# Optimization experiments

Hardware: AMD Instinct MI355X
Metric: run time of the kernel (lower is better)

The kernel has to match this reference:

```python
import jax, jax.numpy as jnp
import numpy as np

E = 16   # num_experts
K = 4    # num_activated_experts
B, S, H, I = 4, 1024, 1024, 2048


def setup_inputs() -> dict:
    key = jax.random.key(0)
    k0, k1, k2, k3 = jax.random.split(key, 4)
    scale = 0.02
    return {
        "hidden_states": jax.random.normal(k0, (B, S, H), jnp.float32),
        "router_w": jax.random.normal(k1, (H, E), jnp.float32) * scale,
        "router_b": jnp.zeros((E,), jnp.float32),
        "w1": jax.random.normal(k2, (E, H, I), jnp.float32) * scale,
        "b1": jnp.zeros((E, I), jnp.float32),
        "w2": jax.random.normal(k3, (E, I, H), jnp.float32) * scale,
        "b2": jnp.zeros((E, H), jnp.float32),
    }


def reference(hidden_states, router_w, router_b, w1, b1, w2, b2):
    b, s, h = hidden_states.shape
    # router: softmax over experts, pick top-k, renormalize top-k weights
    logits = hidden_states @ router_w + router_b            # [B,S,E]
    probs = jax.nn.softmax(logits, axis=-1)
    topw, topi = jax.lax.top_k(probs, K)                    # [B,S,K]
    topw = topw / jnp.sum(topw, axis=-1, keepdims=True)
    # scatter top-k weights into dense per-expert combine weights [B,S,E]
    combine = jnp.sum(
        jax.nn.one_hot(topi, E, dtype=hidden_states.dtype) * topw[..., None],
        axis=2,
    )
    x = hidden_states.reshape(b * s, h)                     # [T,H]
    c = combine.reshape(b * s, E)                           # [T,E]

    def body(acc, expert):
        w1e, b1e, w2e, b2e, ce = expert
        hmid = jax.nn.gelu(x @ w1e + b1e, approximate=False)  # [T,I]
        return acc + (hmid @ w2e + b2e) * ce[:, None], None

    out, _ = jax.lax.scan(body, jnp.zeros_like(x), (w1, b1, w2, b2, c.T))
    return out.reshape(b, s, h)
```

## Files before the change

kernel.cpp:

```cpp
#include <hip/hip_runtime.h>

#define T_TOK 4096
#define H_DIM 1024
#define I_DIM 2048
#define E_NUM 16
#define K_TOP 4
#define BM 128
#define BK 32
#define MAX_TILES 144
#define PAD_PAIRS (MAX_TILES * BM)
#define RW_Q 4104

typedef __attribute__((ext_vector_type(8))) short s16x8;
typedef __attribute__((ext_vector_type(4))) float f32x4;
typedef __attribute__((ext_vector_type(4))) unsigned short u16x4;
typedef __attribute__((ext_vector_type(8))) unsigned short u16x8;

__device__ __forceinline__ unsigned short f2bf(float f) {
  unsigned u = __float_as_uint(f);
  u += 0x7fffu + ((u >> 16) & 1u);
  return (unsigned short)(u >> 16);
}

__device__ __forceinline__ void mfma_bf16(const s16x8& a, const s16x8& b, f32x4& c) {
  asm("v_mfma_f32_16x16x32_bf16 %0, %1, %2, %0" : "+v"(c) : "v"(a), "v"(b));
}

__device__ __forceinline__ void gld16(const void* g, void* l) {
  __builtin_amdgcn_global_load_lds(
      (const __attribute__((address_space(1))) unsigned int*)g,
      (__attribute__((address_space(3))) unsigned int*)l, 16, 0, 0);
}

__global__ __launch_bounds__(256) void cvt_kernel(const float* __restrict__ x,
                                                  unsigned short* __restrict__ xb) {
  size_t i = ((size_t)blockIdx.x * 256 + threadIdx.x) * 8;
  f32x4 a = *(const f32x4*)(x + i);
  f32x4 b = *(const f32x4*)(x + i + 4);
  u16x8 o;
  o[0] = f2bf(a[0]); o[1] = f2bf(a[1]); o[2] = f2bf(a[2]); o[3] = f2bf(a[3]);
  o[4] = f2bf(b[0]); o[5] = f2bf(b[1]); o[6] = f2bf(b[2]); o[7] = f2bf(b[3]);
  *(u16x8*)(xb + i) = o;
}

__global__ __launch_bounds__(256) void router_kernel(
    const float* __restrict__ x, const float* __restrict__ rw,
    const float* __restrict__ rb, int* __restrict__ topi,
    float* __restrict__ topw, int* __restrict__ counts) {
  __shared__ float rws[4 * RW_Q];
  const int tid = threadIdx.x;
  for (int idx = tid * 4; idx < H_DIM * E_NUM; idx += 256 * 4) {
    f32x4 v = *(const f32x4*)(rw + idx);
    int h = idx >> 4, e0 = idx & 15;
    *(f32x4*)&rws[(h >> 8) * RW_Q + (h & 255) * 16 + e0] = v;
  }
  __syncthreads();
  const int w = tid >> 6, l = tid & 63;
  const int e = l & 15, q = l >> 4;
  const float rbe = rb[e];
  const float* ldsb = &rws[q * RW_Q + e];
#pragma unroll
  for (int i = 0; i < 4; ++i) {
    const int t = blockIdx.x * 16 + w * 4 + i;
    const float* xr = x + (size_t)t * H_DIM + (q << 8);
    float acc = 0.f;
#pragma unroll 8
    for (int hh = 0; hh < 256; hh += 4) {
      f32x4 xv = *(const f32x4*)(xr + hh);
      acc += xv[0] * ldsb[(hh + 0) * 16];
      acc += xv[1] * ldsb[(hh + 1) * 16];
      acc += xv[2] * ldsb[(hh + 2) * 16];
      acc += xv[3] * ldsb[(hh + 3) * 16];
    }
    acc += __shfl_xor(acc, 16);
    acc += __shfl_xor(acc, 32);
    float logit = acc + rbe;
    float m = logit;
    m = fmaxf(m, __shfl_xor(m, 1));
    m = fmaxf(m, __shfl_xor(m, 2));
    m = fmaxf(m, __shfl_xor(m, 4));
    m = fmaxf(m, __shfl_xor(m, 8));
    float ex = expf(logit - m);
    int rank = 0;
    const int b16 = l & 48;
#pragma unroll
    for (int j = 0; j < 16; ++j) {
      float vj = __shfl(ex, b16 + j);
      rank += (vj > ex) || (vj == ex && j < e);
    }
    float sel = (rank < K_TOP) ? ex : 0.f;
    float subs = sel;
    subs += __shfl_xor(subs, 1);
    subs += __shfl_xor(subs, 2);
    subs += __shfl_xor(subs, 4);
    subs += __shfl_xor(subs, 8);
    if (q == 0 && rank < K_TOP) {
      topi[t * K_TOP + rank] = e;
      topw[t * K_TOP + rank] = ex / subs;
      atomicAdd(&counts[e], 1);
    }
  }
}

__global__ void scan_kernel(const int* __restrict__ counts, int* padBase,
                            int* tileExpert, int* tileStart, int* nTiles,
                            int* cursor) {
  if (threadIdx.x != 0 || blockIdx.x != 0) return;
  int base = 0, nt = 0;
  for (int e = 0; e < E_NUM; ++e) {
    padBase[e] = base;
    cursor[e] = 0;
    int tc = (counts[e] + BM - 1) >> 7;
    for (int i = 0; i < tc; ++i) {
      tileExpert[nt] = e;
      tileStart[nt] = base + (i << 7);
      ++nt;
    }
    base += tc << 7;
  }
  nTiles[0] = nt;
}

__global__ __launch_bounds__(256) void scatter_kernel(
    const int* __restrict__ topi, const float* __restrict__ topw,
    const int* __restrict__ padBase, int* __restrict__ cursor,
    int* __restrict__ pairTok, float* __restrict__ pairW,
    int* __restrict__ pairPos) {
  int t = blockIdx.x * 256 + threadIdx.x;
  if (t >= T_TOK) return;
#pragma unroll
  for (int k = 0; k < K_TOP; ++k) {
    int e = topi[t * K_TOP + k];
    int pos = atomicAdd(&cursor[e], 1);
    int idx = padBase[e] + pos;
    pairTok[idx] = t;
    pairW[idx] = topw[t * K_TOP + k];
    pairPos[t * K_TOP + k] = idx;
  }
}

__global__ __launch_bounds__(256) void transpose_kernel(
    const float* __restrict__ src, unsigned short* __restrict__ dst, int R,
    int C) {
  size_t es = (size_t)R * C;
  src += es * blockIdx.z;
  dst += es * blockIdx.z;
  int r0 = blockIdx.y * 64, c0 = blockIdx.x * 64;
  __shared__ float tle[64][65];
  int rr = threadIdx.x >> 4, cc = (threadIdx.x & 15) * 4;
#pragma unroll
  for (int i = 0; i < 4; ++i) {
    f32x4 v = *(const f32x4*)(src + (size_t)(r0 + rr + 16 * i) * C + c0 + cc);
    tle[rr + 16 * i][cc + 0] = v[0];
    tle[rr + 16 * i][cc + 1] = v[1];
    tle[rr + 16 * i][cc + 2] = v[2];
    tle[rr + 16 * i][cc + 3] = v[3];
  }
  __syncthreads();
#pragma unroll
  for (int i = 0; i < 4; ++i) {
    int oc = c0 + rr + 16 * i;
    u16x4 o;
    o[0] = f2bf(tle[cc + 0][rr + 16 * i]);
    o[1] = f2bf(tle[cc + 1][rr + 16 * i]);
    o[2] = f2bf(tle[cc + 2][rr + 16 * i]);
    o[3] = f2bf(tle[cc + 3][rr + 16 * i]);
    *(u16x4*)(dst + (size_t)oc * R + r0 + cc) = o;
  }
}

__global__ __launch_bounds__(256, 4) void gemm1_kernel(
    const unsigned short* __restrict__ xb, const unsigned short* __restrict__ w1t,
    const float* __restrict__ b1, unsigned short* __restrict__ hmid,
    const int* __restrict__ pairTok, const int* __restrict__ tileExpert,
    const int* __restrict__ tileStart, const int* __restrict__ nTiles) {
  const int bid = blockIdx.x;
  const int lin = (bid & 7) * ((16 * MAX_TILES) >> 3) + (bid >> 3);
  const int tx = lin & 15, ty = lin >> 4;
  if (ty >= nTiles[0]) return;
  const int e = tileExpert[ty];
  const int tsp = tileStart[ty];
  const int n0 = tx * 128;
  __shared__ unsigned short As[2][BM * BK];
  __shared__ unsigned short Bs[2][BM * BK];
  const int tid = threadIdx.x, w = tid >> 6, l = tid & 63;
  const int rbase = w * 16 + (l >> 2);
  const int segp = (l & 3) ^ ((l >> 3) & 3);
  int tok0 = pairTok[tsp + rbase];
  if (tok0 < 0) tok0 = 0;
  int tok1 = pairTok[tsp + rbase + 64];
  if (tok1 < 0) tok1 = 0;
  const char* gA0 = (const char*)(xb + (size_t)tok0 * H_DIM) + segp * 16;
  const char* gA1 = (const char*)(xb + (size_t)tok1 * H_DIM) + segp * 16;
  const unsigned short* wbase = w1t + (size_t)e * I_DIM * H_DIM;
  const char* gB0 = (const char*)(wbase + (size_t)(n0 + rbase) * H_DIM) + segp * 16;
  const char* gB1 = (const char*)(wbase + (size_t)(n0 + rbase + 64) * H_DIM) + segp * 16;

  f32x4 acc[4][4];
#pragma unroll
  for (int m = 0; m < 4; ++m)
#pragma unroll
    for (int n = 0; n < 4; ++n) acc[m][n] = f32x4{0.f, 0.f, 0.f, 0.f};

  const int wr = w >> 1, wc = w & 1, lrow = l & 15, g = l >> 4;
  const int gs = g ^ ((l >> 1) & 3);
  const int NK = H_DIM / BK;

  gld16(gA0, &As[0][w * 512]);
  gld16(gA1, &As[0][2048 + w * 512]);
  gld16(gB0, &Bs[0][w * 512]);
  gld16(gB1, &Bs[0][2048 + w * 512]);

  for (int kt = 0; kt < NK; ++kt) {
    __syncthreads();
    if (kt + 1 < NK) {
      const int kb = (kt + 1) * 64;
      const int nb = (kt + 1) & 1;
      gld16(gA0 + kb, &As[nb][w * 512]);
      gld16(gA1 + kb, &As[nb][2048 + w * 512]);
      gld16(gB0 + kb, &Bs[nb][w * 512]);
      gld16(gB1 + kb, &Bs[nb][2048 + w * 512]);
    }
    const int cb = kt & 1;
    const s16x8* Ap = (const s16x8*)As[cb];
    const s16x8* Bp = (const s16x8*)Bs[cb];
    s16x8 av[4], bv[4];
#pragma unroll
    for (int m = 0; m < 4; ++m) av[m] = Ap[(wr * 64 + m * 16 + lrow) * 4 + gs];
#pragma unroll
    for (int n = 0; n < 4; ++n) bv[n] = Bp[(wc * 64 + n * 16 + lrow) * 4 + gs];
#pragma unroll
    for (int m = 0; m < 4; ++m)
#pragma unroll
      for (int n = 0; n < 4; ++n) mfma_bf16(av[m], bv[n], acc[m][n]);
  }

  const float* b1e = b1 + (size_t)e * I_DIM;
#pragma unroll
  for (int m = 0; m < 4; ++m) {
    const int rw0 = wr * 64 + m * 16 + g * 4;
#pragma unroll
    for (int n = 0; n < 4; ++n) {
      const int col = n0 + wc * 64 + n * 16 + lrow;
      const float bb = b1e[col];
      f32x4 v = acc[m][n];
#pragma unroll
      for (int j = 0; j < 4; ++j) {
        const int p = tsp + rw0 + j;
        float xv = v[j] + bb;
        float y = 0.7978845608028654f * (xv + 0.044715f * xv * xv * xv);
        float ey = __expf(2.f * y);
        float th = 1.f - 2.f / (ey + 1.f);
        float ge = 0.5f * xv * (1.f + th);
        hmid[(size_t)p * I_DIM + col] = f2bf(ge);
      }
    }
  }
}

__global__ __launch_bounds__(256, 4) void gemm2_kernel(
    const unsigned short* __restrict__ hmid,
    const unsigned short* __restrict__ w2t, const float* __restrict__ b2,
    float* __restrict__ out, unsigned short* __restrict__ pairOut,
    const int* __restrict__ pairTok, const float* __restrict__ pairW,
    const int* __restrict__ tileExpert, const int* __restrict__ tileStart,
    const int* __restrict__ nTiles, int usePairOut) {
  const int bid = blockIdx.x;
  const int lin = (bid & 7) * ((8 * MAX_TILES) >> 3) + (bid >> 3);
  const int tx = lin & 7, ty = lin >> 3;
  if (ty >= nTiles[0]) return;
  const int e = tileExpert[ty];
  const int tsp = tileStart[ty];
  const int n0 = tx * 128;
  __shared__ unsigned short As[2][BM * BK];
  __shared__ unsigned short Bs[2][BM * BK];
  const int tid = threadIdx.x, w = tid >> 6, l = tid & 63;
  const int rbase = w * 16 + (l >> 2);
  const int segp = (l & 3) ^ ((l >> 3) & 3);
  const char* gA0 = (const char*)(hmid + (size_t)(tsp + rbase) * I_DIM) + segp * 16;
  const char* gA1 = (const char*)(hmid + (size_t)(tsp + rbase + 64) * I_DIM) + segp * 16;
  const unsigned short* wbase = w2t + (size_t)e * H_DIM * I_DIM;
  const char* gB0 = (const char*)(wbase + (size_t)(n0 + rbase) * I_DIM) + segp * 16;
  const char* gB1 = (const char*)(wbase + (size_t)(n0 + rbase + 64) * I_DIM) + segp * 16;

  f32x4 acc[4][4];
#pragma unroll
  for (int m = 0; m < 4; ++m)
#pragma unroll
    for (int n = 0; n < 4; ++n) acc[m][n] = f32x4{0.f, 0.f, 0.f, 0.f};

  const int wr = w >> 1, wc = w & 1, lrow = l & 15, g = l >> 4;
  const int gs = g ^ ((l >> 1) & 3);
  const int NK = I_DIM / BK;

  gld16(gA0, &As[0][w * 512]);
  gld16(gA1, &As[0][2048 + w * 512]);
  gld16(gB0, &Bs[0][w * 512]);
  gld16(gB1, &Bs[0][2048 + w * 512]);

  for (int kt = 0; kt < NK; ++kt) {
    __syncthreads();
    if (kt + 1 < NK) {
      const int kb = (kt + 1) * 64;
      const int nb = (kt + 1) & 1;
      gld16(gA0 + kb, &As[nb][w * 512]);
      gld16(gA1 + kb, &As[nb][2048 + w * 512]);
      gld16(gB0 + kb, &Bs[nb][w * 512]);
      gld16(gB1 + kb, &Bs[nb][2048 + w * 512]);
    }
    const int cb = kt & 1;
    const s16x8* Ap = (const s16x8*)As[cb];
    const s16x8* Bp = (const s16x8*)Bs[cb];
    s16x8 av[4], bv[4];
#pragma unroll
    for (int m = 0; m < 4; ++m) av[m] = Ap[(wr * 64 + m * 16 + lrow) * 4 + gs];
#pragma unroll
    for (int n = 0; n < 4; ++n) bv[n] = Bp[(wc * 64 + n * 16 + lrow) * 4 + gs];
#pragma unroll
    for (int m = 0; m < 4; ++m)
#pragma unroll
      for (int n = 0; n < 4; ++n) mfma_bf16(av[m], bv[n], acc[m][n]);
  }

  if (usePairOut) {
#pragma unroll
    for (int m = 0; m < 4; ++m) {
      const int rw0 = wr * 64 + m * 16 + g * 4;
#pragma unroll
      for (int n = 0; n < 4; ++n) {
        const int col = n0 + wc * 64 + n * 16 + lrow;
        f32x4 v = acc[m][n];
#pragma unroll
        for (int j = 0; j < 4; ++j)
          pairOut[(size_t)(tsp + rw0 + j) * H_DIM + col] = f2bf(v[j]);
      }
    }
  } else {
    const float* b2e = b2 + (size_t)e * H_DIM;
#pragma unroll
    for (int m = 0; m < 4; ++m) {
      const int rw0 = wr * 64 + m * 16 + g * 4;
#pragma unroll
      for (int j = 0; j < 4; ++j) {
        const int p = tsp + rw0 + j;
        const int tok = pairTok[p];
        if (tok < 0) continue;
        const float pw = pairW[p];
        float* orow = out + (size_t)tok * H_DIM;
#pragma unroll
        for (int n = 0; n < 4; ++n) {
          const int col = n0 + wc * 64 + n * 16 + lrow;
          float val = (acc[m][n][j] + b2e[col]) * pw;
          atomicAdd(orow + col, val);
        }
      }
    }
  }
}

__global__ __launch_bounds__(256) void combine_kernel(
    const unsigned short* __restrict__ pairOut, const int* __restrict__ pairPos,
    const int* __restrict__ topi, const float* __restrict__ topw,
    const float* __restrict__ b2, float* __restrict__ out) {
  const int t = blockIdx.x * 2 + (threadIdx.x >> 7);
  const int c0 = (threadIdx.x & 127) * 8;
  float o[8];
#pragma unroll
  for (int j = 0; j < 8; ++j) o[j] = 0.f;
#pragma unroll
  for (int k = 0; k < K_TOP; ++k) {
    const int e = topi[t * K_TOP + k];
    const float pw = topw[t * K_TOP + k];
    const int pos = pairPos[t * K_TOP + k];
    u16x8 v = *(const u16x8*)(pairOut + (size_t)pos * H_DIM + c0);
    const float* b2r = b2 + (size_t)e * H_DIM + c0;
#pragma unroll
    for (int j = 0; j < 8; ++j) {
      float hv = __uint_as_float((unsigned)v[j] << 16);
      o[j] += pw * (hv + b2r[j]);
    }
  }
  float* orow = out + (size_t)t * H_DIM + c0;
  *(f32x4*)orow = f32x4{o[0], o[1], o[2], o[3]};
  *(f32x4*)(orow + 4) = f32x4{o[4], o[5], o[6], o[7]};
}

extern "C" void kernel_launch(void* const* d_in, const int* in_sizes, int n_in,
                              void* d_out, int out_size, void* d_ws,
                              size_t ws_size, hipStream_t stream) {
  const float* x = (const float*)d_in[0];
  const float* rw = (const float*)d_in[1];
  const float* rb = (const float*)d_in[2];
  const float* w1 = (const float*)d_in[3];
  const float* b1 = (const float*)d_in[4];
  const float* w2 = (const float*)d_in[5];
  const float* b2 = (const float*)d_in[6];
  float* out = (float*)d_out;
  char* ws = (char*)d_ws;

  const size_t xbSz = (size_t)T_TOK * H_DIM * 2;
  const size_t poSz = (size_t)PAD_PAIRS * H_DIM * 2;
  const size_t wtSz = (size_t)E_NUM * H_DIM * I_DIM * 2;
  const size_t hmSz = (size_t)PAD_PAIRS * I_DIM * 2;
  const size_t smallSz = (size_t)T_TOK * K_TOP * 4 * 3
                         + (size_t)PAD_PAIRS * 4 * 2
                         + 64 * 3 + MAX_TILES * 4 * 2 + 64;
  const size_t richTotal = poSz + wtSz + hmSz + smallSz;
  const size_t poorTotal = xbSz + wtSz + hmSz + smallSz;
  const int rich = ws_size >= richTotal;
  if (!rich && ws_size < poorTotal) return;

  size_t off = 0;
  unsigned short* xb = (unsigned short*)(ws + off);
  unsigned short* pairOut = (unsigned short*)(ws + off);
  off += rich ? poSz : xbSz;
  unsigned short* wT = (unsigned short*)(ws + off);
  off += wtSz;
  unsigned short* hmid = (unsigned short*)(ws + off);
  off += hmSz;
  int* topi = (int*)(ws + off);      off += (size_t)T_TOK * K_TOP * 4;
  float* topw = (float*)(ws + off);  off += (size_t)T_TOK * K_TOP * 4;
  int* pairPos = (int*)(ws + off);   off += (size_t)T_TOK * K_TOP * 4;
  int* pairTok = (int*)(ws + off);   off += (size_t)PAD_PAIRS * 4;
  float* pairW = (float*)(ws + off); off += (size_t)PAD_PAIRS * 4;
  int* counts = (int*)(ws + off);    off += 64;
  int* cursor = (int*)(ws + off);    off += 64;
  int* padBase = (int*)(ws + off);   off += 64;
  int* tileExpert = (int*)(ws + off); off += MAX_TILES * 4;
  int* tileStart = (int*)(ws + off);  off += MAX_TILES * 4;
  int* nTiles = (int*)(ws + off);     off += 64;

  hipMemsetAsync(counts, 0, 64, stream);
  hipMemsetAsync(pairTok, 0xFF, (size_t)PAD_PAIRS * 4, stream);
  if (!rich) hipMemsetAsync(out, 0, (size_t)T_TOK * H_DIM * 4, stream);

  cvt_kernel<<<T_TOK * H_DIM / (256 * 8), 256, 0, stream>>>(x, xb);
  router_kernel<<<T_TOK / 16, 256, 0, stream>>>(x, rw, rb, topi, topw, counts);
  scan_kernel<<<1, 64, 0, stream>>>(counts, padBase, tileExpert, tileStart,
                                    nTiles, cursor);
  scatter_kernel<<<T_TOK / 256, 256, 0, stream>>>(topi, topw, padBase, cursor,
                                                  pairTok, pairW, pairPos);
  transpose_kernel<<<dim3(I_DIM / 64, H_DIM / 64, E_NUM), 256, 0, stream>>>(
      w1, wT, H_DIM, I_DIM);
  gemm1_kernel<<<16 * MAX_TILES, 256, 0, stream>>>(
      xb, wT, b1, hmid, pairTok, tileExpert, tileStart, nTiles);
  transpose_kernel<<<dim3(H_DIM / 64, I_DIM / 64, E_NUM), 256, 0, stream>>>(
      w2, wT, I_DIM, H_DIM);
  gemm2_kernel<<<8 * MAX_TILES, 256, 0, stream>>>(
      hmid, wT, b2, out, pairOut, pairTok, pairW, tileExpert, tileStart, nTiles,
      rich);
  if (rich)
    combine_kernel<<<T_TOK / 2, 256, 0, stream>>>(pairOut, pairPos, topi, topw,
                                                  b2, out);
}
```

Measured before the change: 432.4 us.

## Drop scan kernel via inline tile mapping and split-K gemm2 into two partial buffers

Removes the single-thread scan kernel. Each gemm block and the scatter kernel now derive their expert and tile start directly from the expert counts, which saves one serial launch. When the workspace is large enough, gemm2 is split along K into two halves. Each half writes a bf16 partial result into its own buffer, and the combine kernel sums the two. This doubles the number of gemm2 blocks for better occupancy, at the cost of an extra partial-output write and read and an added bf16 rounding step.

Result: faster. 420.2 us (-2.8%).

```diff
diff --git a/kernel.cpp b/kernel.cpp
--- a/kernel.cpp
+++ b/kernel.cpp
@@ -30,6 +30,21 @@
   __builtin_amdgcn_global_load_lds(
       (const __attribute__((address_space(1))) unsigned int*)g,
       (__attribute__((address_space(3))) unsigned int*)l, 16, 0, 0);
+}
+
+__device__ __forceinline__ int tile_map(const int* counts, int ty, int* tsp) {
+  int e = -1, acc = 0, base = 0;
+#pragma unroll
+  for (int ee = 0; ee < E_NUM; ++ee) {
+    int tc = (counts[ee] + 127) >> 7;
+    if (ty >= acc && ty < acc + tc) {
+      e = ee;
+      *tsp = base + ((ty - acc) << 7);
+    }
+    acc += tc;
+    base += tc << 7;
+  }
+  return e;
 }
 
 __global__ __launch_bounds__(256) void cvt_kernel(const float* __restrict__ x,
@@ -102,30 +117,18 @@
   }
 }
 
-__global__ void scan_kernel(const int* __restrict__ counts, int* padBase,
-                            int* tileExpert, int* tileStart, int* nTiles,
-                            int* cursor) {
-  if (threadIdx.x != 0 || blockIdx.x != 0) return;
-  int base = 0, nt = 0;
-  for (int e = 0; e < E_NUM; ++e) {
-    padBase[e] = base;
-    cursor[e] = 0;
-    int tc = (counts[e] + BM - 1) >> 7;
-    for (int i = 0; i < tc; ++i) {
-      tileExpert[nt] = e;
-      tileStart[nt] = base + (i << 7);
-      ++nt;
-    }
-    base += tc << 7;
-  }
-  nTiles[0] = nt;
-}
-
 __global__ __launch_bounds__(256) void scatter_kernel(
     const int* __restrict__ topi, const float* __restrict__ topw,
-    const int* __restrict__ padBase, int* __restrict__ cursor,
+    const int* __restrict__ counts, int* __restrict__ cursor,
     int* __restrict__ pairTok, float* __restrict__ pairW,
     int* __restrict__ pairPos) {
+  int padBase[E_NUM];
+  int base = 0;
+#pragma unroll
+  for (int ee = 0; ee < E_NUM; ++ee) {
+    padBase[ee] = base;
+    base += ((counts[ee] + 127) >> 7) << 7;
+  }
   int t = blockIdx.x * 256 + threadIdx.x;
   if (t >= T_TOK) return;
 #pragma unroll
@@ -172,14 +175,13 @@
 __global__ __launch_bounds__(256, 4) void gemm1_kernel(
     const unsigned short* __restrict__ xb, const unsigned short* __restrict__ w1t,
     const float* __restrict__ b1, unsigned short* __restrict__ hmid,
-    const int* __restrict__ pairTok, const int* __restrict__ tileExpert,
-    const int* __restrict__ tileStart, const int* __restrict__ nTiles) {
+    const int* __restrict__ pairTok, const int* __restrict__ counts) {
   const int bid = blockIdx.x;
-  const int lin = (bid & 7) * ((16 * MAX_TILES) >> 3) + (bid >> 3);
+  const int lin = (bid & 7) * 288 + (bid >> 3);
   const int tx = lin & 15, ty = lin >> 4;
-  if (ty >= nTiles[0]) return;
-  const int e = tileExpert[ty];
-  const int tsp = tileStart[ty];
+  int tsp = 0;
+  const int e = tile_map(counts, ty, &tsp);
+  if (e < 0) return;
   const int n0 = tx * 128;
   __shared__ unsigned short As[2][BM * BK];
   __shared__ unsigned short Bs[2][BM * BK];
@@ -261,27 +263,34 @@
 __global__ __launch_bounds__(256, 4) void gemm2_kernel(
     const unsigned short* __restrict__ hmid,
     const unsigned short* __restrict__ w2t, const float* __restrict__ b2,
-    float* __restrict__ out, unsigned short* __restrict__ pairOut,
-    const int* __restrict__ pairTok, const float* __restrict__ pairW,
-    const int* __restrict__ tileExpert, const int* __restrict__ tileStart,
-    const int* __restrict__ nTiles, int usePairOut) {
+    float* __restrict__ out, unsigned short* __restrict__ poA,
+    unsigned short* __restrict__ poB, const int* __restrict__ pairTok,
+    const float* __restrict__ pairW, const int* __restrict__ counts, int mode) {
   const int bid = blockIdx.x;
-  const int lin = (bid & 7) * ((8 * MAX_TILES) >> 3) + (bid >> 3);
-  const int tx = lin & 7, ty = lin >> 3;
-  if (ty >= nTiles[0]) return;
-  const int e = tileExpert[ty];
-  const int tsp = tileStart[ty];
+  const int nchunk = (mode == 2) ? 288 : 144;
+  const int lin = (bid & 7) * nchunk + (bid >> 3);
+  const int kh = (mode == 2) ? (lin & 1) : 0;
+  const int tx = (mode == 2) ? ((lin >> 1) & 7) : (lin & 7);
+  const int ty = (mode == 2) ? (lin >> 4) : (lin >> 3);
+  int tsp = 0;
+  const int e = tile_map(counts, ty, &tsp);
+  if (e < 0) return;
   const int n0 = tx * 128;
   __shared__ unsigned short As[2][BM * BK];
   __shared__ unsigned short Bs[2][BM * BK];
   const int tid = threadIdx.x, w = tid >> 6, l = tid & 63;
   const int rbase = w * 16 + (l >> 2);
   const int segp = (l & 3) ^ ((l >> 3) & 3);
-  const char* gA0 = (const char*)(hmid + (size_t)(tsp + rbase) * I_DIM) + segp * 16;
-  const char* gA1 = (const char*)(hmid + (size_t)(tsp + rbase + 64) * I_DIM) + segp * 16;
+  const size_t koff = (size_t)kh * 2048;
+  const char* gA0 =
+      (const char*)(hmid + (size_t)(tsp + rbase) * I_DIM) + segp * 16 + koff;
+  const char* gA1 =
+      (const char*)(hmid + (size_t)(tsp + rbase + 64) * I_DIM) + segp * 16 + koff;
   const unsigned short* wbase = w2t + (size_t)e * H_DIM * I_DIM;
-  const char* gB0 = (const char*)(wbase + (size_t)(n0 + rbase) * I_DIM) + segp * 16;
-  const char* gB1 = (const char*)(wbase + (size_t)(n0 + rbase + 64) * I_DIM) + segp * 16;
+  const char* gB0 =
+      (const char*)(wbase + (size_t)(n0 + rbase) * I_DIM) + segp * 16 + koff;
+  const char* gB1 =
+      (const char*)(wbase + (size_t)(n0 + rbase + 64) * I_DIM) + segp * 16 + koff;
 
   f32x4 acc[4][4];
 #pragma unroll
@@ -291,7 +300,7 @@
 
   const int wr = w >> 1, wc = w & 1, lrow = l & 15, g = l >> 4;
   const int gs = g ^ ((l >> 1) & 3);
-  const int NK = I_DIM / BK;
+  const int NK = (mode == 2) ? 32 : 64;
 
   gld16(gA0, &As[0][w * 512]);
   gld16(gA1, &As[0][2048 + w * 512]);
@@ -322,7 +331,8 @@
       for (int n = 0; n < 4; ++n) mfma_bf16(av[m], bv[n], acc[m][n]);
   }
 
-  if (usePairOut) {
+  if (mode >= 1) {
+    unsigned short* po = (kh == 0) ? poA : poB;
 #pragma unroll
     for (int m = 0; m < 4; ++m) {
       const int rw0 = wr * 64 + m * 16 + g * 4;
@@ -332,7 +342,7 @@
         f32x4 v = acc[m][n];
 #pragma unroll
         for (int j = 0; j < 4; ++j)
-          pairOut[(size_t)(tsp + rw0 + j) * H_DIM + col] = f2bf(v[j]);
+          po[(size_t)(tsp + rw0 + j) * H_DIM + col] = f2bf(v[j]);
       }
     }
   } else {
@@ -359,9 +369,10 @@
 }
 
 __global__ __launch_bounds__(256) void combine_kernel(
-    const unsigned short* __restrict__ pairOut, const int* __restrict__ pairPos,
-    const int* __restrict__ topi, const float* __restrict__ topw,
-    const float* __restrict__ b2, float* __restrict__ out) {
+    const unsigned short* __restrict__ poA, const unsigned short* __restrict__ poB,
+    const int* __restrict__ pairPos, const int* __restrict__ topi,
+    const float* __restrict__ topw, const float* __restrict__ b2,
+    float* __restrict__ out, int nbuf) {
   const int t = blockIdx.x * 2 + (threadIdx.x >> 7);
   const int c0 = (threadIdx.x & 127) * 8;
   float o[8];
@@ -372,11 +383,14 @@
     const int e = topi[t * K_TOP + k];
     const float pw = topw[t * K_TOP + k];
     const int pos = pairPos[t * K_TOP + k];
-    u16x8 v = *(const u16x8*)(pairOut + (size_t)pos * H_DIM + c0);
+    u16x8 va = *(const u16x8*)(poA + (size_t)pos * H_DIM + c0);
+    u16x8 vb;
+    if (nbuf == 2) vb = *(const u16x8*)(poB + (size_t)pos * H_DIM + c0);
     const float* b2r = b2 + (size_t)e * H_DIM + c0;
 #pragma unroll
     for (int j = 0; j < 8; ++j) {
-      float hv = __uint_as_float((unsigned)v[j] << 16);
+      float hv = __uint_as_float((unsigned)va[j] << 16);
+      if (nbuf == 2) hv += __uint_as_float((unsigned)vb[j] << 16);
       o[j] += pw * (hv + b2r[j]);
     }
   }
@@ -404,16 +418,21 @@
   const size_t hmSz = (size_t)PAD_PAIRS * I_DIM * 2;
   const size_t smallSz = (size_t)T_TOK * K_TOP * 4 * 3
                          + (size_t)PAD_PAIRS * 4 * 2
-                         + 64 * 3 + MAX_TILES * 4 * 2 + 64;
-  const size_t richTotal = poSz + wtSz + hmSz + smallSz;
-  const size_t poorTotal = xbSz + wtSz + hmSz + smallSz;
-  const int rich = ws_size >= richTotal;
-  if (!rich && ws_size < poorTotal) return;
+                         + 128;
+  const size_t needSplit = poSz * 2 + wtSz + hmSz + smallSz;
+  const size_t needRich = poSz + wtSz + hmSz + smallSz;
+  const size_t needPoor = xbSz + wtSz + hmSz + smallSz;
+  int mode = 0;
+  if (ws_size >= needSplit) mode = 2;
+  else if (ws_size >= needRich) mode = 1;
+  else if (ws_size < needPoor) return;
 
   size_t off = 0;
   unsigned short* xb = (unsigned short*)(ws + off);
-  unsigned short* pairOut = (unsigned short*)(ws + off);
-  off += rich ? poSz : xbSz;
+  unsigned short* poA = (unsigned short*)(ws + off);
+  off += (mode >= 1) ? poSz : xbSz;
+  unsigned short* poB = (unsigned short*)(ws + off);
+  if (mode == 2) off += poSz;
   unsigned short* wT = (unsigned short*)(ws + off);
   off += wtSz;
   unsigned short* hmid = (unsigned short*)(ws + off);
@@ -425,31 +444,24 @@
   float* pairW = (float*)(ws + off); off += (size_t)PAD_PAIRS * 4;
   int* counts = (int*)(ws + off);    off += 64;
   int* cursor = (int*)(ws + off);    off += 64;
-  int* padBase = (int*)(ws + off);   off += 64;
-  int* tileExpert = (int*)(ws + off); off += MAX_TILES * 4;
-  int* tileStart = (int*)(ws + off);  off += MAX_TILES * 4;
-  int* nTiles = (int*)(ws + off);     off += 64;
-
-  hipMemsetAsync(counts, 0, 64, stream);
+
+  hipMemsetAsync(counts, 0, 128, stream);
   hipMemsetAsync(pairTok, 0xFF, (size_t)PAD_PAIRS * 4, stream);
-  if (!rich) hipMemsetAsync(out, 0, (size_t)T_TOK * H_DIM * 4, stream);
+  if (mode == 0) hipMemsetAsync(out, 0, (size_t)T_TOK * H_DIM * 4, stream);
 
   cvt_kernel<<<T_TOK * H_DIM / (256 * 8), 256, 0, stream>>>(x, xb);
   router_kernel<<<T_TOK / 16, 256, 0, stream>>>(x, rw, rb, topi, topw, counts);
-  scan_kernel<<<1, 64, 0, stream>>>(counts, padBase, tileExpert, tileStart,
-                                    nTiles, cursor);
-  scatter_kernel<<<T_TOK / 256, 256, 0, stream>>>(topi, topw, padBase, cursor,
+  scatter_kernel<<<T_TOK / 256, 256, 0, stream>>>(topi, topw, counts, cursor,
                                                   pairTok, pairW, pairPos);
   transpose_kernel<<<dim3(I_DIM / 64, H_DIM / 64, E_NUM), 256, 0, stream>>>(
       w1, wT, H_DIM, I_DIM);
-  gemm1_kernel<<<16 * MAX_TILES, 256, 0, stream>>>(
-      xb, wT, b1, hmid, pairTok, tileExpert, tileStart, nTiles);
+  gemm1_kernel<<<16 * MAX_TILES, 256, 0, stream>>>(xb, wT, b1, hmid, pairTok,
+                                                   counts);
   transpose_kernel<<<dim3(H_DIM / 64, I_DIM / 64, E_NUM), 256, 0, stream>>>(
       w2, wT, I_DIM, H_DIM);
-  gemm2_kernel<<<8 * MAX_TILES, 256, 0, stream>>>(
-      hmid, wT, b2, out, pairOut, pairTok, pairW, tileExpert, tileStart, nTiles,
-      rich);
-  if (rich)
-    combine_kernel<<<T_TOK / 2, 256, 0, stream>>>(pairOut, pairPos, topi, topw,
-                                                  b2, out);
-}
+  gemm2_kernel<<<(mode == 2 ? 16 : 8) * MAX_TILES, 256, 0, stream>>>(
+      hmid, wT, b2, out, poA, poB, pairTok, pairW, counts, mode);
+  if (mode >= 1)
+    combine_kernel<<<T_TOK / 2, 256, 0, stream>>>(poA, poB, pairPos, topi, topw,
+                                                  b2, out, mode);
+}
```
